# Optimization experiments

Measured on AMD Instinct MI355X. Metric: run time of the kernel, lower is better.

## Reference

```python
import jax, jax.numpy as jnp
from jax import lax
import numpy as np
import math

N, T, H, PD = 1024, 32, 256, 256
E, DT, SD = 2 * H, H // 16, 16  # mamba expand, dt_rank, state_dim
TAU = 1.0

def _xavier(k, shape):
    s = math.sqrt(6.0 / (shape[0] + shape[1]))
    return jax.random.uniform(k, shape, minval=-s, maxval=s, dtype=jnp.float32)

def setup_inputs() -> dict:
    key = jax.random.key(0)
    ks = jax.random.split(key, 40)
    adj = (jax.random.uniform(ks[0], (T, N, N)) < 0.02).astype(jnp.float32)
    p = {
        'adj': adj,
        # input SpatialLayer (pos_dim -> H)
        'msg1_w': _xavier(ks[1], (PD, H)), 'msg1_b': jnp.zeros(H),
        'upd1_w': _xavier(ks[2], (PD + H, H)), 'upd1_b': jnp.zeros(H),
        'ln1_g': jnp.ones(H), 'ln1_b': jnp.zeros(H),
        # second SpatialLayer (H -> H)
        'msg2_w': _xavier(ks[3], (H, H)), 'msg2_b': jnp.zeros(H),
        'upd2_w': _xavier(ks[4], (2 * H, H)), 'upd2_b': jnp.zeros(H),
        'ln2_g': jnp.ones(H), 'ln2_b': jnp.zeros(H),
        # MambaBlock
        'mb_ln_g': jnp.ones(H), 'mb_ln_b': jnp.zeros(H),
        'in_w': _xavier(ks[5], (H, 2 * E)), 'in_b': jnp.zeros(2 * E),
        'delta_w': _xavier(ks[6], (E, DT)), 'delta_b': jnp.zeros(DT),
        'dt_w': _xavier(ks[7], (DT, E)), 'dt_b': jnp.zeros(E),
        'Bp_w': _xavier(ks[8], (E, SD)), 'Bp_b': jnp.zeros(SD),
        'Cp_w': _xavier(ks[9], (E, SD)), 'Cp_b': jnp.zeros(SD),
        'A_log': -jnp.exp(0.1 * jax.random.normal(ks[10], (E, SD))),
        'D_vec': jnp.zeros(E),
        'out_w': _xavier(ks[11], (E, H)), 'out_b': jnp.zeros(H),
        # LateEdgeGateHead
        'q_w': _xavier(ks[12], (H, H)), 'k_w': _xavier(ks[13], (H, H)),
        'gate_bias': jnp.float32(-1.0),
    }
    return p

def _layernorm(x, g, b, eps=1e-5):
    mu = jnp.mean(x, -1, keepdims=True)
    var = jnp.mean(jnp.square(x - mu), -1, keepdims=True)
    return (x - mu) / jnp.sqrt(var + eps) * g + b

def _sincos_pe(n, d):
    pos = jnp.arange(n, dtype=jnp.float32)[:, None]
    div = jnp.exp(jnp.arange(0, d, 2, dtype=jnp.float32) * (-math.log(10000.0) / d))
    ang = pos * div  # [n, d/2]
    return jnp.stack([jnp.sin(ang), jnp.cos(ang)], axis=-1).reshape(n, d)

def reference(adj, msg1_w, msg1_b, upd1_w, upd1_b, ln1_g, ln1_b,
              msg2_w, msg2_b, upd2_w, upd2_b, ln2_g, ln2_b,
              mb_ln_g, mb_ln_b, in_w, in_b, delta_w, delta_b, dt_w, dt_b,
              Bp_w, Bp_b, Cp_w, Cp_b, A_log, D_vec, out_w, out_b,
              q_w, k_w, gate_bias):
    pe = _sincos_pe(N, PD)  # [N, PD]
    # --- spatial layer 1 (shared pe across time) ---
    m1 = pe @ msg1_w + msg1_b                                   # [N, H]
    agg1 = jnp.einsum('tij,jh->tih', adj, m1)                   # [T, N, H]
    x = jnp.concatenate([jnp.broadcast_to(pe, (T, N, PD)), agg1], -1)
    x = _layernorm(jax.nn.relu(x @ upd1_w + upd1_b), ln1_g, ln1_b)
    # --- spatial layer 2 ---
    m2 = x @ msg2_w + msg2_b
    agg2 = jnp.einsum('tij,tjh->tih', adj, m2)
    x = jnp.concatenate([x, agg2], -1)
    x = _layernorm(jax.nn.relu(x @ upd2_w + upd2_b), ln2_g, ln2_b)  # [T, N, H]
    # --- Mamba over time, batch = nodes ---
    seq = jnp.transpose(x, (1, 0, 2))                           # [N, T, H]
    res = seq
    xn = _layernorm(seq, mb_ln_g, mb_ln_b)
    xp = xn @ in_w + in_b
    x1, gate = jnp.split(xp, 2, axis=-1)                        # [N, T, E] each
    x1 = jax.nn.silu(x1)
    delta = jax.nn.softplus((x1 @ delta_w + delta_b) @ dt_w + dt_b)  # [N, T, E]
    Bm = x1 @ Bp_w + Bp_b                                       # [N, T, SD]
    Cm = x1 @ Cp_w + Cp_b
    A = -jnp.exp(A_log)                                         # [E, SD]
    def step(h, inp):
        xt, dt_, bt, ct = inp                                   # [N,E],[N,E],[N,SD],[N,SD]
        A_disc = jnp.exp(dt_[:, :, None] * A)                   # [N, E, SD]
        h = A_disc * h + dt_[:, :, None] * bt[:, None, :] * xt[:, :, None]
        yt = jnp.sum(ct[:, None, :] * h, -1)                    # [N, E]
        return h, yt
    h0 = jnp.zeros((N, E, SD), dtype=seq.dtype)
    xs = (jnp.swapaxes(x1, 0, 1), jnp.swapaxes(delta, 0, 1),
          jnp.swapaxes(Bm, 0, 1), jnp.swapaxes(Cm, 0, 1))
    _, ys = lax.scan(step, h0, xs)                              # [T, N, E]
    y = jnp.swapaxes(ys, 0, 1) + x1 * D_vec
    y = y * jax.nn.silu(gate)
    mb_out = y @ out_w + out_b + res                            # [N, T, H]
    outs = jnp.transpose(mb_out, (1, 0, 2))                     # [T, N, H]
    # --- late gate head per timestep ---
    q = outs @ q_w
    k = outs @ k_w
    scores = jnp.einsum('tnh,tmh->tnm', q, k) / (math.sqrt(H) * max(TAU, 1e-6))
    logits = scores + gate_bias
    probs = jax.nn.sigmoid(logits)
    return outs, probs, logits
```

## Files before the change

kernel.cpp:

```cpp
#include <hip/hip_runtime.h>
#include <hip/hip_bf16.h>

typedef __hip_bfloat16 bf16;
typedef short s16x8 __attribute__((ext_vector_type(8)));
typedef float f32x4 __attribute__((ext_vector_type(4)));

#define T_  32
#define N_  1024
#define H_  256
#define E_  512
#define SD_ 16

static const long MBYTE = 1024L * 1024L;

__device__ __forceinline__ float b2f(bf16 v){ return __bfloat162float(v); }
__device__ __forceinline__ bf16  f2b(float v){ return __float2bfloat16(v); }

#define G2L16(gp, lp) __builtin_amdgcn_global_load_lds( \
    (const __attribute__((address_space(1))) void*)(const void*)(gp), \
    (__attribute__((address_space(3))) void*)(void*)(lp), 16, 0, 0)

struct TDesc { const float* src; int K; int N; bf16* dst; int ldT; };
struct PrepArgs {
    TDesc t[13];
    bf16* pe;
    const float* pa; const float* pb; const float* pc; float* po;
    const float* adj; unsigned short* IDX; int* CNT;
};

__global__ __launch_bounds__(256) void prep_kernel(PrepArgs P){
    int z = blockIdx.z;
    int tid = threadIdx.x;
    if (z < 13) {
        const TDesc d = P.t[z];
        int k0 = blockIdx.x * 32, n0 = blockIdx.y * 32;
        if (k0 >= d.K || n0 >= d.N) return;
        __shared__ float S[32][33];
        int r = tid >> 3, c4 = (tid & 7) * 4;
        #pragma unroll
        for (int u = 0; u < 4; ++u) {
            int k = k0 + r, n = n0 + c4 + u;
            S[r][c4 + u] = (k < d.K && n < d.N) ? d.src[(long)k * d.N + n] : 0.0f;
        }
        __syncthreads();
        int n = n0 + (tid >> 3);
        #pragma unroll
        for (int u = 0; u < 4; ++u) {
            int k = k0 + (tid & 7) * 4 + u;
            if (n < d.N && k < d.K) d.dst[(long)n * d.ldT + k] = f2b(S[(tid & 7) * 4 + u][tid >> 3]);
        }
    } else if (z == 13) {
        int n = blockIdx.y * 32 + blockIdx.x;
        int dd = tid;
        int i2 = (dd >> 1) * 2;
        float div = __expf((float)i2 * (-9.210340371976184f / 256.0f));
        float ang = (float)n * div;
        P.pe[n * 256 + dd] = f2b((dd & 1) ? __cosf(ang) : __sinf(ang));
    } else if (z == 14) {
        if (blockIdx.x || blockIdx.y) return;
        if (tid < 16) P.po[tid] = P.pa[tid];
        else if (tid < 32) P.po[tid] = P.pb[tid - 16];
        else if (tid < 48) P.po[tid] = P.pc[tid - 32];
    } else {
        int r = (z - 15) * 1024 + blockIdx.y * 32 + blockIdx.x;
        const float* arow = P.adj + ((long)r << 10);
        __shared__ int wcnt[4];
        int wv = tid >> 6, lane = tid & 63;
        int total = 0;
        unsigned short* out = P.IDX + (long)r * 128;
        #pragma unroll
        for (int u = 0; u < 4; ++u) {
            float av = arow[u * 256 + tid];
            unsigned long long mask = __ballot(av != 0.0f);
            if (lane == 0) wcnt[wv] = __popcll(mask);
            __syncthreads();
            int base = total;
            for (int w2 = 0; w2 < wv; ++w2) base += wcnt[w2];
            if (av != 0.0f) {
                int pos = base + __popcll(mask & ((1ull << lane) - 1ull));
                if (pos < 128) out[pos] = (unsigned short)(u * 256 + tid);
            }
            total += wcnt[0] + wcnt[1] + wcnt[2] + wcnt[3];
            __syncthreads();
        }
        if (tid == 0) P.CNT[r] = total < 128 ? total : 128;
    }
}

template<int OP, bool NTF>
__global__ __launch_bounds__(256) void mfma_gemm128(
    const bf16* __restrict__ A, int lda,
    const bf16* BT0, const bf16* BT1, int ldbt0, int ldbt1,
    float* Cf0, float* Cf1, bf16* Cb0, bf16* Cb1, int ldc,
    int K, const float* bias0, const float* bias1, const bf16* resb)
{
    int z = blockIdx.z;
    const bf16* BT = z ? BT1 : BT0;
    int ldbt = z ? ldbt1 : ldbt0;
    float* Cf = z ? Cf1 : Cf0;
    bf16*  Cb = z ? Cb1 : Cb0;
    const float* bias = z ? bias1 : bias0;

    __shared__ short As[4096];
    __shared__ short Bs[4096];
    int tid = threadIdx.x;
    int w = tid >> 6, l = tid & 63;
    int wr = w >> 1, wc = w & 1;
    long row0 = (long)blockIdx.y * 128, col0 = (long)blockIdx.x * 128;
    const short* Ag = (const short*)A + row0 * lda;
    const short* Bg = (const short*)BT + col0 * ldbt;
    int sr = w * 16 + (l >> 2);
    int sc = (l & 3) * 8;
    short* lA = As + w * 512 + l * 8;
    short* lB = Bs + w * 512 + l * 8;
    f32x4 acc[4][4] = {};
    for (int k0 = 0; k0 < K; k0 += 32) {
        G2L16(Ag + (long)sr * lda + k0 + sc, lA);
        G2L16(Ag + (long)(sr + 64) * lda + k0 + sc, lA + 2048);
        G2L16(Bg + (long)sr * ldbt + k0 + sc, lB);
        G2L16(Bg + (long)(sr + 64) * ldbt + k0 + sc, lB + 2048);
        __syncthreads();
        s16x8 af[4], bf[4];
        #pragma unroll
        for (int f = 0; f < 4; ++f) {
            af[f] = *(const s16x8*)&As[(wr * 64 + f * 16 + (l & 15)) * 32 + (l >> 4) * 8];
            bf[f] = *(const s16x8*)&Bs[(wc * 64 + f * 16 + (l & 15)) * 32 + (l >> 4) * 8];
        }
        #pragma unroll
        for (int fm = 0; fm < 4; ++fm)
            #pragma unroll
            for (int fn = 0; fn < 4; ++fn)
                acc[fm][fn] = __builtin_amdgcn_mfma_f32_16x16x32_bf16(af[fm], bf[fn], acc[fm][fn], 0, 0, 0);
        __syncthreads();
    }
    #pragma unroll
    for (int fm = 0; fm < 4; ++fm) {
        int er = (int)row0 + wr * 64 + fm * 16 + (l >> 4) * 4;
        #pragma unroll
        for (int fn = 0; fn < 4; ++fn) {
            int ec = (int)col0 + wc * 64 + fn * 16 + (l & 15);
            float bb = bias ? bias[ec] : 0.0f;
            #pragma unroll
            for (int rg = 0; rg < 4; ++rg) {
                long idx = (long)(er + rg) * ldc + ec;
                float v = acc[fm][fn][rg] + bb;
                if (resb) v += b2f(resb[idx]);
                if (OP == 1) v = v / (1.0f + __expf(-v));
                if (Cf) { if (NTF) __builtin_nontemporal_store(v, &Cf[idx]); else Cf[idx] = v; }
                if (Cb) Cb[idx] = f2b(v);
            }
        }
    }
}

__global__ __launch_bounds__(256) void score_mfma128(
    const bf16* __restrict__ Q, const bf16* __restrict__ Km,
    float* __restrict__ probs, float* __restrict__ logits,
    const float* __restrict__ gbp)
{
    int t = blockIdx.z;
    const short* Ag = (const short*)(Q  + (long)t * N_ * 256) + (long)blockIdx.y * 128 * 256;
    const short* Bg = (const short*)(Km + (long)t * N_ * 256) + (long)blockIdx.x * 128 * 256;
    __shared__ short As[4096];
    __shared__ short Bs[4096];
    int tid = threadIdx.x;
    int w = tid >> 6, l = tid & 63;
    int wr = w >> 1, wc = w & 1;
    int sr = w * 16 + (l >> 2);
    int sc = (l & 3) * 8;
    short* lA = As + w * 512 + l * 8;
    short* lB = Bs + w * 512 + l * 8;
    f32x4 acc[4][4] = {};
    for (int k0 = 0; k0 < 256; k0 += 32) {
        G2L16(Ag + (long)sr * 256 + k0 + sc, lA);
        G2L16(Ag + (long)(sr + 64) * 256 + k0 + sc, lA + 2048);
        G2L16(Bg + (long)sr * 256 + k0 + sc, lB);
        G2L16(Bg + (long)(sr + 64) * 256 + k0 + sc, lB + 2048);
        __syncthreads();
        s16x8 af[4], bf[4];
        #pragma unroll
        for (int f = 0; f < 4; ++f) {
            af[f] = *(const s16x8*)&As[(wr * 64 + f * 16 + (l & 15)) * 32 + (l >> 4) * 8];
            bf[f] = *(const s16x8*)&Bs[(wc * 64 + f * 16 + (l & 15)) * 32 + (l >> 4) * 8];
        }
        #pragma unroll
        for (int fm = 0; fm < 4; ++fm)
            #pragma unroll
            for (int fn = 0; fn < 4; ++fn)
                acc[fm][fn] = __builtin_amdgcn_mfma_f32_16x16x32_bf16(af[fm], bf[fn], acc[fm][fn], 0, 0, 0);
        __syncthreads();
    }
    float gb = gbp[0];
    long tbase = (long)t * N_ * N_;
    int row0 = blockIdx.y * 128, col0 = blockIdx.x * 128;
    #pragma unroll
    for (int fm = 0; fm < 4; ++fm) {
        int er = row0 + wr * 64 + fm * 16 + (l >> 4) * 4;
        #pragma unroll
        for (int fn = 0; fn < 4; ++fn) {
            int ec = col0 + wc * 64 + fn * 16 + (l & 15);
            #pragma unroll
            for (int rg = 0; rg < 4; ++rg) {
                float zz = acc[fm][fn][rg] * 0.0625f + gb;
                long idx = tbase + (long)(er + rg) * N_ + ec;
                __builtin_nontemporal_store(zz, &logits[idx]);
                __builtin_nontemporal_store(1.0f / (1.0f + __expf(-zz)), &probs[idx]);
            }
        }
    }
}

__global__ __launch_bounds__(256) void mfma_gemm64(
    const bf16* __restrict__ A, int lda,
    const bf16* __restrict__ BT, int ldbt,
    float* __restrict__ Cf, int ldc,
    int M, int N, int K, const float* __restrict__ bias)
{
    __shared__ short As[64][40];
    __shared__ short Bs[64][40];
    int tid = threadIdx.x;
    int w = tid >> 6, l = tid & 63;
    int row0 = blockIdx.y * 64, col0 = blockIdx.x * 64;
    int sr = tid >> 2, sk = (tid & 3) * 8;
    const short* Ag = (const short*)A;
    const short* Bg = (const short*)BT;
    f32x4 acc[4] = {};
    for (int k0 = 0; k0 < K; k0 += 32) {
        *(s16x8*)&As[sr][sk] = *(const s16x8*)(Ag + (long)(row0 + sr) * lda + k0 + sk);
        int bn = col0 + sr;
        s16x8 bv = {};
        if (bn < N) bv = *(const s16x8*)(Bg + (long)bn * ldbt + k0 + sk);
        *(s16x8*)&Bs[sr][sk] = bv;
        __syncthreads();
        s16x8 a = *(const s16x8*)&As[w * 16 + (l & 15)][(l >> 4) * 8];
        #pragma unroll
        for (int ct = 0; ct < 4; ++ct) {
            s16x8 b = *(const s16x8*)&Bs[ct * 16 + (l & 15)][(l >> 4) * 8];
            acc[ct] = __builtin_amdgcn_mfma_f32_16x16x32_bf16(a, b, acc[ct], 0, 0, 0);
        }
        __syncthreads();
    }
    int er = row0 + w * 16 + (l >> 4) * 4;
    int ec = l & 15;
    #pragma unroll
    for (int ct = 0; ct < 4; ++ct) {
        int gc = col0 + ct * 16 + ec;
        if (gc >= N) continue;
        float bb = bias ? bias[gc] : 0.0f;
        #pragma unroll
        for (int rg = 0; rg < 4; ++rg)
            Cf[(long)(er + rg) * ldc + gc] = acc[ct][rg] + bb;
    }
}

__global__ __launch_bounds__(256) void agg_gather(
    const unsigned short* __restrict__ IDX, const int* __restrict__ CNT,
    const bf16* __restrict__ Bm, long tstride,
    bf16* __restrict__ out, int old, int ooff)
{
    int r = blockIdx.x;
    int t = r >> 10;
    const bf16* B = Bm + (long)t * tstride;
    __shared__ unsigned short sidx[128];
    int tid = threadIdx.x;
    int cnt = CNT[r];
    if (tid < 128) sidx[tid] = IDX[(long)r * 128 + tid];
    __syncthreads();
    float a0 = 0.0f, a1 = 0.0f, a2 = 0.0f, a3 = 0.0f;
    int k = 0;
    for (; k + 4 <= cnt; k += 4) {
        float v0 = b2f(B[(long)sidx[k]     * 256 + tid]);
        float v1 = b2f(B[(long)sidx[k + 1] * 256 + tid]);
        float v2 = b2f(B[(long)sidx[k + 2] * 256 + tid]);
        float v3 = b2f(B[(long)sidx[k + 3] * 256 + tid]);
        a0 += v0; a1 += v1; a2 += v2; a3 += v3;
    }
    for (; k < cnt; ++k) a0 += b2f(B[(long)sidx[k] * 256 + tid]);
    out[(long)r * old + ooff + tid] = f2b((a0 + a1) + (a2 + a3));
}

__global__ __launch_bounds__(256) void row_ln1(
    const float* __restrict__ in, const float* __restrict__ addf,
    const float* __restrict__ g, const float* __restrict__ b,
    bf16* __restrict__ out, int rows)
{
    int wv = threadIdx.x >> 6, lane = threadIdx.x & 63;
    int row = blockIdx.x * 4 + wv;
    if (row >= rows) return;
    const float* p = in + (long)row * 256 + lane * 4;
    const float* q = addf + (long)(row & 1023) * 256 + lane * 4;
    float v[4];
    #pragma unroll
    for (int u = 0; u < 4; ++u) v[u] = fmaxf(p[u] + q[u], 0.0f);
    float s = v[0] + v[1] + v[2] + v[3];
    #pragma unroll
    for (int o = 32; o >= 1; o >>= 1) s += __shfl_xor(s, o, 64);
    float mu = s * (1.0f / 256.0f);
    float d0 = v[0]-mu, d1 = v[1]-mu, d2 = v[2]-mu, d3 = v[3]-mu;
    float sq = d0*d0 + d1*d1 + d2*d2 + d3*d3;
    #pragma unroll
    for (int o = 32; o >= 1; o >>= 1) sq += __shfl_xor(sq, o, 64);
    float rs = rsqrtf(sq * (1.0f / 256.0f) + 1e-5f);
    bf16* o = out + (long)row * 512 + lane * 4;
    #pragma unroll
    for (int u = 0; u < 4; ++u)
        o[u] = f2b((v[u] - mu) * rs * g[lane * 4 + u] + b[lane * 4 + u]);
}

__global__ __launch_bounds__(256) void dbl_ln(
    const float* __restrict__ in,
    const float* __restrict__ g2, const float* __restrict__ b2,
    const float* __restrict__ gm, const float* __restrict__ bm,
    bf16* __restrict__ X2b, bf16* __restrict__ XNb, int rows)
{
    int wv = threadIdx.x >> 6, lane = threadIdx.x & 63;
    int row = blockIdx.x * 4 + wv;
    if (row >= rows) return;
    const float* p = in + (long)row * 256 + lane * 4;
    float v[4];
    #pragma unroll
    for (int u = 0; u < 4; ++u) v[u] = fmaxf(p[u], 0.0f);
    float s = v[0] + v[1] + v[2] + v[3];
    #pragma unroll
    for (int o = 32; o >= 1; o >>= 1) s += __shfl_xor(s, o, 64);
    float mu = s * (1.0f / 256.0f);
    float sq = 0.0f;
    #pragma unroll
    for (int u = 0; u < 4; ++u) { float d = v[u] - mu; sq += d * d; }
    #pragma unroll
    for (int o = 32; o >= 1; o >>= 1) sq += __shfl_xor(sq, o, 64);
    float rs = rsqrtf(sq * (1.0f / 256.0f) + 1e-5f);
    float o1[4];
    bf16* qx = X2b + (long)row * 256 + lane * 4;
    #pragma unroll
    for (int u = 0; u < 4; ++u) {
        o1[u] = (v[u] - mu) * rs * g2[lane * 4 + u] + b2[lane * 4 + u];
        qx[u] = f2b(o1[u]);
    }
    float s2 = o1[0] + o1[1] + o1[2] + o1[3];
    #pragma unroll
    for (int o = 32; o >= 1; o >>= 1) s2 += __shfl_xor(s2, o, 64);
    float mu2 = s2 * (1.0f / 256.0f);
    float sq2 = 0.0f;
    #pragma unroll
    for (int u = 0; u < 4; ++u) { float d = o1[u] - mu2; sq2 += d * d; }
    #pragma unroll
    for (int o = 32; o >= 1; o >>= 1) sq2 += __shfl_xor(sq2, o, 64);
    float rs2 = rsqrtf(sq2 * (1.0f / 256.0f) + 1e-5f);
    bf16* qn = XNb + (long)row * 256 + lane * 4;
    #pragma unroll
    for (int u = 0; u < 4; ++u)
        qn[u] = f2b((o1[u] - mu2) * rs2 * gm[lane * 4 + u] + bm[lane * 4 + u]);
}

__global__ __launch_bounds__(512) void scan2(
    const bf16* __restrict__ X1,
    bf16* __restrict__ G,
    const float* __restrict__ DBC,
    const bf16* __restrict__ DTwT,
    const float* __restrict__ DTb,
    const float* __restrict__ A_log,
    const float* __restrict__ D_vec)
{
    int n = blockIdx.x;
    int e = threadIdx.x;
    float A[SD_], wdt[SD_];
    #pragma unroll
    for (int s = 0; s < SD_; ++s) A[s] = -__expf(A_log[e * SD_ + s]);
    #pragma unroll
    for (int s = 0; s < SD_; ++s) wdt[s] = b2f(DTwT[e * SD_ + s]);
    float dtb = DTb[e];
    float Dv = D_vec[e];
    float h[SD_];
    #pragma unroll
    for (int s = 0; s < SD_; ++s) h[s] = 0.0f;
    for (int t = 0; t < T_; ++t) {
        long row = (long)t * N_ + n;
        const float* dbc = DBC + row * 48;
        float z = dtb;
        #pragma unroll
        for (int k = 0; k < SD_; ++k) z += dbc[k] * wdt[k];
        float dt = (z > 15.0f) ? z : __logf(1.0f + __expf(z));
        float x1 = b2f(X1[row * (long)E_ + e]);
        float gv = b2f(G[row * (long)E_ + e]);
        float dx = dt * x1;
        float yv = 0.0f;
        #pragma unroll
        for (int s = 0; s < SD_; ++s) {
            h[s] = __expf(dt * A[s]) * h[s] + dx * dbc[16 + s];
            yv += dbc[32 + s] * h[s];
        }
        G[row * (long)E_ + e] = f2b((yv + x1 * Dv) * gv);
    }
}

extern "C" void kernel_launch(void* const* d_in, const int* in_sizes, int n_in,
                              void* d_out, int out_size, void* d_ws, size_t ws_size,
                              hipStream_t stream)
{
    if (ws_size < (size_t)(212 * MBYTE)) return;
    if (n_in != 32 || in_sizes[0] != T_ * N_ * N_ || in_sizes[15] != 256 * 1024) return;

    const float* adj = (const float*)d_in[0];
    const float* P1w = (const float*)d_in[1];
    const float* P1b = (const float*)d_in[2];
    const float* U1w = (const float*)d_in[3];
    const float* U1b = (const float*)d_in[4];
    const float* L1g = (const float*)d_in[5];
    const float* L1b = (const float*)d_in[6];
    const float* P2w = (const float*)d_in[7];
    const float* P2b = (const float*)d_in[8];
    const float* U2w = (const float*)d_in[9];
    const float* U2b = (const float*)d_in[10];
    const float* L2g = (const float*)d_in[11];
    const float* L2b = (const float*)d_in[12];
    const float* MBg = (const float*)d_in[13];
    const float* MBb = (const float*)d_in[14];
    const float* INw = (const float*)d_in[15];
    const float* INb = (const float*)d_in[16];
    const float* DLw = (const float*)d_in[17];
    const float* DLb = (const float*)d_in[18];
    const float* DTw = (const float*)d_in[19];
    const float* DTb = (const float*)d_in[20];
    const float* BPw = (const float*)d_in[21];
    const float* BPb = (const float*)d_in[22];
    const float* CPw = (const float*)d_in[23];
    const float* CPb = (const float*)d_in[24];
    const float* ALg = (const float*)d_in[25];
    const float* DV  = (const float*)d_in[26];
    const float* OWw = (const float*)d_in[27];
    const float* OWb = (const float*)d_in[28];
    const float* QWw = (const float*)d_in[29];
    const float* KWw = (const float*)d_in[30];
    const float* GB  = (const float*)d_in[31];

    char* w = (char*)d_ws;
    float* R0    = (float*)(w + 0);
    bf16*  XCATb = (bf16*)(w + 32 * MBYTE);
    bf16*  AGG1b = (bf16*)(w + 64 * MBYTE);
    bf16*  M2b   = (bf16*)(w + 64 * MBYTE);
    bf16*  OUTb  = (bf16*)(w + 64 * MBYTE);
    bf16*  X1b   = (bf16*)(w + 80 * MBYTE);
    bf16*  Gb    = (bf16*)(w + 112 * MBYTE);
    bf16*  X2b   = (bf16*)(w + 144 * MBYTE);
    bf16*  Qb    = (bf16*)(w + 144 * MBYTE);
    bf16*  Kb    = (bf16*)(w + 160 * MBYTE);
    bf16*  XNb   = (bf16*)(w + 176 * MBYTE);
    float* DBC   = (float*)(w + 192 * MBYTE);
    unsigned short* IDX = (unsigned short*)(w + 198 * MBYTE);
    int*   CNT   = (int*)(w + 206 * MBYTE);
    float* BASE1 = (float*)(w + 207 * MBYTE);
    bf16*  PEb   = (bf16*)(w + 208 * MBYTE);
    bf16*  M1b   = (bf16*)(w + 208 * MBYTE + 524288);
    bf16*  WT    = (bf16*)(w + 209 * MBYTE);
    float* B48   = (float*)(w + 211 * MBYTE);

    bf16* P1wT  = WT + 0;
    bf16* U1wT  = WT + 65536;
    bf16* P2wT  = WT + 196608;
    bf16* U2wT  = WT + 262144;
    bf16* INwT  = WT + 393216;
    bf16* DTwT  = WT + 655360;
    bf16* OWwT  = WT + 663552;
    bf16* QWwT  = WT + 794624;
    bf16* KWwT  = WT + 860160;
    bf16* DBCwT = WT + 925696;

    float* out0       = (float*)d_out;
    float* out_probs  = out0 + (long)T_ * N_ * H_;
    float* out_logits = out_probs + (long)T_ * N_ * N_;

    const int RN = T_ * N_;
    dim3 blk(256);
    const float* fnull = nullptr;
    float* f32null = nullptr;
    bf16*  b16null = nullptr;
    const bf16* cb16null = nullptr;

    PrepArgs P;
    P.t[0]  = {P1w, 256, 256,  P1wT, 256};
    P.t[1]  = {U1w, 512, 256,  U1wT, 512};
    P.t[2]  = {P2w, 256, 256,  P2wT, 256};
    P.t[3]  = {U2w, 512, 256,  U2wT, 512};
    P.t[4]  = {INw, 256, 1024, INwT, 256};
    P.t[5]  = {DTw, 16,  512,  DTwT, 16};
    P.t[6]  = {OWw, 512, 256,  OWwT, 512};
    P.t[7]  = {QWw, 256, 256,  QWwT, 256};
    P.t[8]  = {KWw, 256, 256,  KWwT, 256};
    P.t[9]  = {DLw, 512, 16,   DBCwT, 512};
    P.t[10] = {BPw, 512, 16,   DBCwT + 16 * 512, 512};
    P.t[11] = {CPw, 512, 16,   DBCwT + 32 * 512, 512};
    P.t[12] = {DLw, 1,   1,    DBCwT, 512};
    P.pe = PEb; P.pa = DLb; P.pb = BPb; P.pc = CPb; P.po = B48;
    P.adj = adj; P.IDX = IDX; P.CNT = CNT;
    hipLaunchKernelGGL(prep_kernel, dim3(32, 32, 47), blk, 0, stream, P);

    hipLaunchKernelGGL((mfma_gemm128<0, false>), dim3(2, 8, 2), blk, 0, stream,
                       PEb, 256, P1wT, U1wT, 256, 512,
                       f32null, BASE1, M1b, b16null, 256, 256, P1b, U1b, cb16null);

    hipLaunchKernelGGL(agg_gather, dim3(RN), blk, 0, stream, IDX, CNT, M1b, 0L, AGG1b, 256, 0);

    hipLaunchKernelGGL((mfma_gemm128<0, false>), dim3(2, 256, 1), blk, 0, stream,
                       AGG1b, 256, U1wT + 256, U1wT + 256, 512, 512,
                       R0, f32null, b16null, b16null, 256, 256, fnull, fnull, cb16null);
    hipLaunchKernelGGL(row_ln1, dim3(RN / 4), blk, 0, stream, R0, BASE1, L1g, L1b, XCATb, RN);

    hipLaunchKernelGGL((mfma_gemm128<0, false>), dim3(2, 256, 1), blk, 0, stream,
                       XCATb, 512, P2wT, P2wT, 256, 256,
                       f32null, f32null, M2b, b16null, 256, 256, P2b, fnull, cb16null);

    hipLaunchKernelGGL(agg_gather, dim3(RN), blk, 0, stream, IDX, CNT, M2b,
                       (long)N_ * 256, XCATb, 512, 256);

    hipLaunchKernelGGL((mfma_gemm128<0, false>), dim3(2, 256, 1), blk, 0, stream,
                       XCATb, 512, U2wT, U2wT, 512, 512,
                       R0, f32null, b16null, b16null, 256, 512, U2b, fnull, cb16null);
    hipLaunchKernelGGL(dbl_ln, dim3(RN / 4), blk, 0, stream,
                       R0, L2g, L2b, MBg, MBb, X2b, XNb, RN);

    hipLaunchKernelGGL((mfma_gemm128<1, false>), dim3(4, 256, 2), blk, 0, stream,
                       XNb, 256, INwT, INwT + 512 * 256, 256, 256,
                       f32null, f32null, X1b, Gb, 512, 256, INb, INb + 512, cb16null);

    hipLaunchKernelGGL(mfma_gemm64, dim3(1, 512), blk, 0, stream,
                       X1b, 512, DBCwT, 512, DBC, 48, RN, 48, 512, B48);

    hipLaunchKernelGGL(scan2, dim3(N_), dim3(512), 0, stream,
                       X1b, Gb, DBC, DTwT, DTb, ALg, DV);

    hipLaunchKernelGGL((mfma_gemm128<0, true>), dim3(2, 256, 1), blk, 0, stream,
                       Gb, 512, OWwT, OWwT, 512, 512,
                       out0, f32null, OUTb, b16null, 256, 512, OWb, fnull, X2b);

    hipLaunchKernelGGL((mfma_gemm128<0, false>), dim3(2, 256, 2), blk, 0, stream,
                       OUTb, 256, QWwT, KWwT, 256, 256,
                       f32null, f32null, Qb, Kb, 256, 256, fnull, fnull, cb16null);

    hipLaunchKernelGGL(score_mfma128, dim3(8, 8, T_), blk, 0, stream,
                       Qb, Kb, out_probs, out_logits, GB);
}
```

Before: 558.0 us.

## Use BK=64 with XOR-swizzled LDS tiles and fold score scale into Q weights

Both 128x128 MFMA GEMM kernels now stage 64-wide K slices, twice as much per barrier, using an XOR swizzle on the LDS column index. This halves the number of sync points and is meant to avoid LDS bank conflicts on fragment reads. The 1/sqrt(H) score scale is folded into the transposed Q weight during prep, which removes one multiply per score in the epilogue. In exchange, LDS use per block doubles, which may lower occupancy.

```diff
diff --git a/kernel.cpp b/kernel.cpp
--- a/kernel.cpp
+++ b/kernel.cpp
@@ -20,7 +20,7 @@
     (const __attribute__((address_space(1))) void*)(const void*)(gp), \
     (__attribute__((address_space(3))) void*)(void*)(lp), 16, 0, 0)
 
-struct TDesc { const float* src; int K; int N; bf16* dst; int ldT; };
+struct TDesc { const float* src; int K; int N; bf16* dst; int ldT; float scale; };
 struct PrepArgs {
     TDesc t[13];
     bf16* pe;
@@ -47,7 +47,8 @@
         #pragma unroll
         for (int u = 0; u < 4; ++u) {
             int k = k0 + (tid & 7) * 4 + u;
-            if (n < d.N && k < d.K) d.dst[(long)n * d.ldT + k] = f2b(S[(tid & 7) * 4 + u][tid >> 3]);
+            if (n < d.N && k < d.K)
+                d.dst[(long)n * d.ldT + k] = f2b(S[(tid & 7) * 4 + u][tid >> 3] * d.scale);
         }
     } else if (z == 13) {
         int n = blockIdx.y * 32 + blockIdx.x;
@@ -101,36 +102,42 @@
     bf16*  Cb = z ? Cb1 : Cb0;
     const float* bias = z ? bias1 : bias0;
 
-    __shared__ short As[4096];
-    __shared__ short Bs[4096];
+    __shared__ short As[8192];
+    __shared__ short Bs[8192];
     int tid = threadIdx.x;
     int w = tid >> 6, l = tid & 63;
     int wr = w >> 1, wc = w & 1;
     long row0 = (long)blockIdx.y * 128, col0 = (long)blockIdx.x * 128;
     const short* Ag = (const short*)A + row0 * lda;
     const short* Bg = (const short*)BT + col0 * ldbt;
-    int sr = w * 16 + (l >> 2);
-    int sc = (l & 3) * 8;
+    int strow = w * 8 + (l >> 3);
+    int stcol = ((l & 7) ^ (l >> 3)) * 8;
     short* lA = As + w * 512 + l * 8;
     short* lB = Bs + w * 512 + l * 8;
     f32x4 acc[4][4] = {};
-    for (int k0 = 0; k0 < K; k0 += 32) {
-        G2L16(Ag + (long)sr * lda + k0 + sc, lA);
-        G2L16(Ag + (long)(sr + 64) * lda + k0 + sc, lA + 2048);
-        G2L16(Bg + (long)sr * ldbt + k0 + sc, lB);
-        G2L16(Bg + (long)(sr + 64) * ldbt + k0 + sc, lB + 2048);
-        __syncthreads();
-        s16x8 af[4], bf[4];
-        #pragma unroll
-        for (int f = 0; f < 4; ++f) {
-            af[f] = *(const s16x8*)&As[(wr * 64 + f * 16 + (l & 15)) * 32 + (l >> 4) * 8];
-            bf[f] = *(const s16x8*)&Bs[(wc * 64 + f * 16 + (l & 15)) * 32 + (l >> 4) * 8];
-        }
-        #pragma unroll
-        for (int fm = 0; fm < 4; ++fm)
+    for (int k0 = 0; k0 < K; k0 += 64) {
+        #pragma unroll
+        for (int i = 0; i < 4; ++i) {
+            G2L16(Ag + (long)(strow + i * 32) * lda + k0 + stcol, lA + i * 2048);
+            G2L16(Bg + (long)(strow + i * 32) * ldbt + k0 + stcol, lB + i * 2048);
+        }
+        __syncthreads();
+        #pragma unroll
+        for (int kk = 0; kk < 2; ++kk) {
+            s16x8 af[4], bf[4];
             #pragma unroll
-            for (int fn = 0; fn < 4; ++fn)
-                acc[fm][fn] = __builtin_amdgcn_mfma_f32_16x16x32_bf16(af[fm], bf[fn], acc[fm][fn], 0, 0, 0);
+            for (int f = 0; f < 4; ++f) {
+                int Ra = wr * 64 + f * 16 + (l & 15);
+                af[f] = *(const s16x8*)&As[Ra * 64 + (((kk * 4 + (l >> 4)) ^ (Ra & 7)) * 8)];
+                int Rb = wc * 64 + f * 16 + (l & 15);
+                bf[f] = *(const s16x8*)&Bs[Rb * 64 + (((kk * 4 + (l >> 4)) ^ (Rb & 7)) * 8)];
+            }
+            #pragma unroll
+            for (int fm = 0; fm < 4; ++fm)
+                #pragma unroll
+                for (int fn = 0; fn < 4; ++fn)
+                    acc[fm][fn] = __builtin_amdgcn_mfma_f32_16x16x32_bf16(af[fm], bf[fn], acc[fm][fn], 0, 0, 0);
+        }
         __syncthreads();
     }
     #pragma unroll
@@ -161,33 +168,39 @@
     int t = blockIdx.z;
     const short* Ag = (const short*)(Q  + (long)t * N_ * 256) + (long)blockIdx.y * 128 * 256;
     const short* Bg = (const short*)(Km + (long)t * N_ * 256) + (long)blockIdx.x * 128 * 256;
-    __shared__ short As[4096];
-    __shared__ short Bs[4096];
+    __shared__ short As[8192];
+    __shared__ short Bs[8192];
     int tid = threadIdx.x;
     int w = tid >> 6, l = tid & 63;
     int wr = w >> 1, wc = w & 1;
-    int sr = w * 16 + (l >> 2);
-    int sc = (l & 3) * 8;
+    int strow = w * 8 + (l >> 3);
+    int stcol = ((l & 7) ^ (l >> 3)) * 8;
     short* lA = As + w * 512 + l * 8;
     short* lB = Bs + w * 512 + l * 8;
     f32x4 acc[4][4] = {};
-    for (int k0 = 0; k0 < 256; k0 += 32) {
-        G2L16(Ag + (long)sr * 256 + k0 + sc, lA);
-        G2L16(Ag + (long)(sr + 64) * 256 + k0 + sc, lA + 2048);
-        G2L16(Bg + (long)sr * 256 + k0 + sc, lB);
-        G2L16(Bg + (long)(sr + 64) * 256 + k0 + sc, lB + 2048);
-        __syncthreads();
-        s16x8 af[4], bf[4];
-        #pragma unroll
-        for (int f = 0; f < 4; ++f) {
-            af[f] = *(const s16x8*)&As[(wr * 64 + f * 16 + (l & 15)) * 32 + (l >> 4) * 8];
-            bf[f] = *(const s16x8*)&Bs[(wc * 64 + f * 16 + (l & 15)) * 32 + (l >> 4) * 8];
-        }
-        #pragma unroll
-        for (int fm = 0; fm < 4; ++fm)
+    for (int k0 = 0; k0 < 256; k0 += 64) {
+        #pragma unroll
+        for (int i = 0; i < 4; ++i) {
+            G2L16(Ag + (long)(strow + i * 32) * 256 + k0 + stcol, lA + i * 2048);
+            G2L16(Bg + (long)(strow + i * 32) * 256 + k0 + stcol, lB + i * 2048);
+        }
+        __syncthreads();
+        #pragma unroll
+        for (int kk = 0; kk < 2; ++kk) {
+            s16x8 af[4], bf[4];
             #pragma unroll
-            for (int fn = 0; fn < 4; ++fn)
-                acc[fm][fn] = __builtin_amdgcn_mfma_f32_16x16x32_bf16(af[fm], bf[fn], acc[fm][fn], 0, 0, 0);
+            for (int f = 0; f < 4; ++f) {
+                int Ra = wr * 64 + f * 16 + (l & 15);
+                af[f] = *(const s16x8*)&As[Ra * 64 + (((kk * 4 + (l >> 4)) ^ (Ra & 7)) * 8)];
+                int Rb = wc * 64 + f * 16 + (l & 15);
+                bf[f] = *(const s16x8*)&Bs[Rb * 64 + (((kk * 4 + (l >> 4)) ^ (Rb & 7)) * 8)];
+            }
+            #pragma unroll
+            for (int fm = 0; fm < 4; ++fm)
+                #pragma unroll
+                for (int fn = 0; fn < 4; ++fn)
+                    acc[fm][fn] = __builtin_amdgcn_mfma_f32_16x16x32_bf16(af[fm], bf[fn], acc[fm][fn], 0, 0, 0);
+        }
         __syncthreads();
     }
     float gb = gbp[0];
@@ -201,7 +214,7 @@
             int ec = col0 + wc * 64 + fn * 16 + (l & 15);
             #pragma unroll
             for (int rg = 0; rg < 4; ++rg) {
-                float zz = acc[fm][fn][rg] * 0.0625f + gb;
+                float zz = acc[fm][fn][rg] + gb;
                 long idx = tbase + (long)(er + rg) * N_ + ec;
                 __builtin_nontemporal_store(zz, &logits[idx]);
                 __builtin_nontemporal_store(1.0f / (1.0f + __expf(-zz)), &probs[idx]);
@@ -478,19 +491,19 @@
     const bf16* cb16null = nullptr;
 
     PrepArgs P;
-    P.t[0]  = {P1w, 256, 256,  P1wT, 256};
-    P.t[1]  = {U1w, 512, 256,  U1wT, 512};
-    P.t[2]  = {P2w, 256, 256,  P2wT, 256};
-    P.t[3]  = {U2w, 512, 256,  U2wT, 512};
-    P.t[4]  = {INw, 256, 1024, INwT, 256};
-    P.t[5]  = {DTw, 16,  512,  DTwT, 16};
-    P.t[6]  = {OWw, 512, 256,  OWwT, 512};
-    P.t[7]  = {QWw, 256, 256,  QWwT, 256};
-    P.t[8]  = {KWw, 256, 256,  KWwT, 256};
-    P.t[9]  = {DLw, 512, 16,   DBCwT, 512};
-    P.t[10] = {BPw, 512, 16,   DBCwT + 16 * 512, 512};
-    P.t[11] = {CPw, 512, 16,   DBCwT + 32 * 512, 512};
-    P.t[12] = {DLw, 1,   1,    DBCwT, 512};
+    P.t[0]  = {P1w, 256, 256,  P1wT, 256, 1.0f};
+    P.t[1]  = {U1w, 512, 256,  U1wT, 512, 1.0f};
+    P.t[2]  = {P2w, 256, 256,  P2wT, 256, 1.0f};
+    P.t[3]  = {U2w, 512, 256,  U2wT, 512, 1.0f};
+    P.t[4]  = {INw, 256, 1024, INwT, 256, 1.0f};
+    P.t[5]  = {DTw, 16,  512,  DTwT, 16, 1.0f};
+    P.t[6]  = {OWw, 512, 256,  OWwT, 512, 1.0f};
+    P.t[7]  = {QWw, 256, 256,  QWwT, 256, 0.0625f};
+    P.t[8]  = {KWw, 256, 256,  KWwT, 256, 1.0f};
+    P.t[9]  = {DLw, 512, 16,   DBCwT, 512, 1.0f};
+    P.t[10] = {BPw, 512, 16,   DBCwT + 16 * 512, 512, 1.0f};
+    P.t[11] = {CPw, 512, 16,   DBCwT + 32 * 512, 512, 1.0f};
+    P.t[12] = {DLw, 1,   1,    DBCwT, 512, 1.0f};
     P.pe = PEb; P.pa = DLb; P.pb = BPb; P.pc = CPb; P.po = B48;
     P.adj = adj; P.IDX = IDX; P.CNT = CNT;
     hipLaunchKernelGGL(prep_kernel, dim3(32, 32, 47), blk, 0, stream, P);
```

Result: no change. 553.4 us, median of 2 (-0.8%).
